# Optimization experiments

Measured on AMD Instinct MI355X. Metric: run time of the kernel, lower is better.

Reference implementation:

```python
import jax, jax.numpy as jnp
import numpy as np

N_NODES = 100000
N_EDGES = 640000
D_IN = 128
D_H = 128


def _lin_params(key, fan_in, fan_out):
    kw, kb = jax.random.split(key)
    s = 1.0 / np.sqrt(fan_in)
    W = jax.random.uniform(kw, (fan_in, fan_out), jnp.float32, -s, s)
    b = jax.random.uniform(kb, (fan_out,), jnp.float32, -s, s)
    return W, b


def setup_inputs() -> dict:
    key = jax.random.key(0)
    ks = jax.random.split(key, 9)
    x = jax.random.normal(ks[0], (N_NODES, D_IN), jnp.float32)
    edge_index = jax.random.randint(ks[1], (2, N_EDGES), 0, N_NODES, dtype=jnp.int64)
    W1, b1 = _lin_params(ks[2], D_IN, D_H)
    W2, b2 = _lin_params(ks[3], D_H, D_H)
    W3, b3 = _lin_params(ks[4], D_H, D_H)
    Wg0, bg0 = _lin_params(ks[5], D_H, D_H)
    Wg1, bg1 = _lin_params(ks[6], D_H, D_H)
    Wo, bo = _lin_params(ks[7], D_H, 1)
    return {"x": x, "edge_index": edge_index,
            "W1": W1, "b1": b1, "W2": W2, "b2": b2, "W3": W3, "b3": b3,
            "Wg0": Wg0, "bg0": bg0, "Wg1": Wg1, "bg1": bg1, "Wo": Wo, "bo": bo}


def gcn_conv(x, src, dst, W, b, n_nodes):
    """PyG GCNConv: D^{-1/2} (A+I) D^{-1/2} X W + b (self-loops added, sym norm)."""
    h = x @ W  # [N, F_out]
    # degree of A+I counted on target side (each self-loop adds 1)
    deg = jnp.zeros((n_nodes,), x.dtype).at[dst].add(1.0) + 1.0
    dis = jax.lax.rsqrt(deg)  # deg^{-1/2}
    coef = dis[src] * dis[dst]  # [E]
    agg = jax.ops.segment_sum(h[src] * coef[:, None], dst, num_segments=n_nodes)
    out = agg + h * (dis * dis)[:, None]  # self-loop term
    return out + b


def reference(x, edge_index, W1, b1, W2, b2, W3, b3, Wg0, bg0, Wg1, bg1, Wo, bo):
    src, dst = edge_index[0], edge_index[1]
    n = x.shape[0]
    lrelu = jax.nn.leaky_relu  # slope 0.01, matches torch default
    # feature extractor MLP
    h = lrelu(x @ W1 + b1)
    h = lrelu(h @ W2 + b2)
    h = lrelu(h @ W3 + b3)
    # input GCN
    h = lrelu(gcn_conv(h, src, dst, Wg0, bg0, n))
    # hidden GCN (dropout is identity in eval mode)
    h = lrelu(gcn_conv(h, src, dst, Wg1, bg1, n))
    # output GCN -> scalar per node
    return gcn_conv(h, src, dst, Wo, bo, n)
```

## Files before the change

kernel.cpp:

```cpp
#include <hip/hip_runtime.h>
#include <hip/hip_bf16.h>

#define D_H 128

typedef __attribute__((ext_vector_type(8))) short bf16x8;
typedef __attribute__((ext_vector_type(4))) float f32x4;

__device__ inline void trunc_split(float x, ushort& hi, ushort& lo) {
    uint u = __builtin_bit_cast(uint, x);
    hi = (ushort)(u >> 16);
    float fh = __builtin_bit_cast(float, u & 0xFFFF0000u);
    float fl = x - fh;
    lo = (ushort)(__builtin_bit_cast(uint, fl) >> 16);
}


__global__ __launch_bounds__(256)
void deg_count_int_kernel(const int* __restrict__ dst, int* __restrict__ cnt, int E) {
    int e = blockIdx.x * 256 + threadIdx.x;
    if (e < E) atomicAdd(&cnt[dst[e]], 1);
}

__global__ __launch_bounds__(256)
void scan_blocks_kernel(const int* __restrict__ cnt, int* __restrict__ rowptr,
                        int* __restrict__ aux, int M) {
    __shared__ int sdata[256];
    const int base = blockIdx.x * 1024 + threadIdx.x * 4;
    int v[4];
#pragma unroll
    for (int i = 0; i < 4; ++i) v[i] = (base + i < M) ? cnt[base + i] : 0;
    int tsum = v[0] + v[1] + v[2] + v[3];
    sdata[threadIdx.x] = tsum;
    __syncthreads();
    int val = tsum;
    for (int off = 1; off < 256; off <<= 1) {
        int n = (threadIdx.x >= off) ? sdata[threadIdx.x - off] : 0;
        __syncthreads();
        val += n;
        sdata[threadIdx.x] = val;
        __syncthreads();
    }
    int run = val - tsum;
#pragma unroll
    for (int i = 0; i < 4; ++i) {
        if (base + i < M) rowptr[base + i] = run;
        run += v[i];
    }
    if (threadIdx.x == 255) aux[blockIdx.x] = val;
}

__global__ __launch_bounds__(128)
void scan_aux_kernel(int* __restrict__ aux, int n) {
    __shared__ int s[128];
    int v = (threadIdx.x < n) ? aux[threadIdx.x] : 0;
    s[threadIdx.x] = v;
    __syncthreads();
    int val = v;
    for (int off = 1; off < 128; off <<= 1) {
        int nn = (threadIdx.x >= off) ? s[threadIdx.x - off] : 0;
        __syncthreads();
        val += nn;
        s[threadIdx.x] = val;
        __syncthreads();
    }
    if (threadIdx.x < n) aux[threadIdx.x] = val - v;
}

__global__ __launch_bounds__(256)
void scan_add_kernel(int* __restrict__ rowptr, int* __restrict__ cursor,
                     const int* __restrict__ aux, const int* __restrict__ cnt,
                     float* __restrict__ dis, int M) {
    int i = blockIdx.x * 256 + threadIdx.x;
    if (i >= M) return;
    int v = rowptr[i] + aux[i >> 10];
    rowptr[i] = v;
    cursor[i] = v;
    dis[i] = rsqrtf((float)cnt[i] + 1.0f);
}

__global__ __launch_bounds__(256)
void scatter_kernel(const int* __restrict__ src, const int* __restrict__ dst,
                    const float* __restrict__ dis, int* __restrict__ cursor,
                    int* __restrict__ es, float* __restrict__ ces, int E) {
    int e = blockIdx.x * 256 + threadIdx.x;
    if (e >= E) return;
    int s = src[e], d = dst[e];
    int pos = atomicAdd(&cursor[d], 1);
    es[pos] = s;
    ces[pos] = dis[s];
}

__global__ __launch_bounds__(256)
void wprep_kernel(const float* __restrict__ W1, const float* __restrict__ W2,
                  const float* __restrict__ W3, const float* __restrict__ W4,
                  const float* __restrict__ W5, ushort* __restrict__ imgs) {
    int w = blockIdx.x >> 6;
    int e = (blockIdx.x & 63) * 256 + threadIdx.x;
    const float* W = w == 0 ? W1 : w == 1 ? W2 : w == 2 ? W3 : w == 3 ? W4 : W5;
    int k = e >> 7, n = e & 127;
    ushort hi, lo;
    trunc_split(W[e], hi, lo);
    ushort* img = imgs + (size_t)w * 34816;
    img[n * 136 + k]         = hi;
    img[17408 + n * 136 + k] = lo;
}

__global__ __launch_bounds__(512, 4)
void fused_mlp4_kernel(const float* __restrict__ X, const ushort* __restrict__ imgs,
                       const float* __restrict__ b1, const float* __restrict__ b2,
                       const float* __restrict__ b3, float* __restrict__ Y, int M) {
    __shared__ ushort sW[34816];
    float* sAct = (float*)sW;

    const int tid  = threadIdx.x;
    const int lane = tid & 63;
    const int wv   = tid >> 6;
    const int bn   = lane & 15;
    const int g    = lane >> 4;
    const int kof  = g * 8;
    const int row0 = blockIdx.x * 128;
    const int lrow = wv * 16 + bn;

    uint4 wreg[9];
    {
        const uint4* g4 = (const uint4*)imgs;
#pragma unroll
        for (int j = 0; j < 9; ++j) {
            int c = j * 512 + tid;
            wreg[j] = (c < 4352) ? g4[c] : make_uint4(0, 0, 0, 0);
        }
    }

    bf16x8 ahi[4], alo[4];
    {
        const int arow = row0 + lrow;
        const bool ok = arow < M;
        const float* ap = X + (size_t)arow * 128 + kof;
#pragma unroll
        for (int kb = 0; kb < 4; ++kb) {
            float f[8];
            if (ok) {
                float4 f0 = *(const float4*)(ap + kb * 32);
                float4 f1 = *(const float4*)(ap + kb * 32 + 4);
                f[0] = f0.x; f[1] = f0.y; f[2] = f0.z; f[3] = f0.w;
                f[4] = f1.x; f[5] = f1.y; f[6] = f1.z; f[7] = f1.w;
            } else {
#pragma unroll
                for (int e = 0; e < 8; ++e) f[e] = 0.f;
            }
            bf16x8 h, l;
#pragma unroll
            for (int e = 0; e < 8; ++e) {
                ushort hb, lb;
                trunc_split(f[e], hb, lb);
                h[e] = (short)hb; l[e] = (short)lb;
            }
            ahi[kb] = h; alo[kb] = l;
        }
    }

    f32x4 acc[8];
    for (int t = 0; t < 4; ++t) {
        {
            uint4* s4 = (uint4*)sW;
#pragma unroll
            for (int j = 0; j < 9; ++j) {
                int c = j * 512 + tid;
                if (c < 4352) s4[c] = wreg[j];
            }
        }
        __syncthreads();

        if (t < 3) {
            const uint4* g4 = (const uint4*)(imgs + (size_t)(t + 1) * 34816);
#pragma unroll
            for (int j = 0; j < 9; ++j) {
                int c = j * 512 + tid;
                wreg[j] = (c < 4352) ? g4[c] : make_uint4(0, 0, 0, 0);
            }
        }

#pragma unroll
        for (int nt = 0; nt < 8; ++nt) acc[nt] = (f32x4){0.f, 0.f, 0.f, 0.f};
#pragma unroll
        for (int kb = 0; kb < 4; ++kb) {
#pragma unroll
            for (int nt = 0; nt < 8; ++nt) {
                const ushort* ph = &sW[(nt * 16 + bn) * 136 + kb * 32 + kof];
                bf16x8 bh = *(const bf16x8*)ph;
                bf16x8 bl = *(const bf16x8*)(ph + 17408);
                acc[nt] = __builtin_amdgcn_mfma_f32_16x16x32_bf16(ahi[kb], bh, acc[nt], 0, 0, 0);
                acc[nt] = __builtin_amdgcn_mfma_f32_16x16x32_bf16(alo[kb], bh, acc[nt], 0, 0, 0);
                acc[nt] = __builtin_amdgcn_mfma_f32_16x16x32_bf16(ahi[kb], bl, acc[nt], 0, 0, 0);
            }
        }

        if (t < 3) {
            __syncthreads();
            const float* bias = t == 0 ? b1 : t == 1 ? b2 : b3;
#pragma unroll
            for (int nt = 0; nt < 8; ++nt) {
                int col = nt * 16 + bn;
                float bc = bias[col];
#pragma unroll
                for (int i = 0; i < 4; ++i) {
                    float v = acc[nt][i] + bc;
                    v = v > 0.f ? v : 0.01f * v;
                    sAct[(wv * 16 + g * 4 + i) * 132 + col] = v;
                }
            }
#pragma unroll
            for (int kb = 0; kb < 4; ++kb) {
                float4 f0 = *(const float4*)&sAct[lrow * 132 + kb * 32 + kof];
                float4 f1 = *(const float4*)&sAct[lrow * 132 + kb * 32 + kof + 4];
                float f[8] = {f0.x, f0.y, f0.z, f0.w, f1.x, f1.y, f1.z, f1.w};
                bf16x8 h, l;
#pragma unroll
                for (int e = 0; e < 8; ++e) {
                    ushort hb, lb;
                    trunc_split(f[e], hb, lb);
                    h[e] = (short)hb; l[e] = (short)lb;
                }
                ahi[kb] = h; alo[kb] = l;
            }
            __syncthreads();
        } else {
#pragma unroll
            for (int nt = 0; nt < 8; ++nt) {
                int col = nt * 16 + bn;
#pragma unroll
                for (int i = 0; i < 4; ++i) {
                    int row = row0 + wv * 16 + g * 4 + i;
                    if (row < M) Y[(size_t)row * 128 + col] = acc[nt][i];
                }
            }
        }
    }
}

__global__ __launch_bounds__(512, 4)
void gemm128_mfma_kernel(const float* __restrict__ X, const ushort* __restrict__ img,
                         float* __restrict__ Y, int M) {
    __shared__ ushort sB[34816];

    const int tid  = threadIdx.x;
    const int lane = tid & 63;
    const int wv   = tid >> 6;
    const int bn   = lane & 15;
    const int g    = lane >> 4;
    const int kof  = g * 8;
    const int row0 = blockIdx.x * 128;
    const int arow = row0 + wv * 16 + bn;

    uint4 wreg[9];
    {
        const uint4* g4 = (const uint4*)img;
#pragma unroll
        for (int j = 0; j < 9; ++j) {
            int c = j * 512 + tid;
            wreg[j] = (c < 4352) ? g4[c] : make_uint4(0, 0, 0, 0);
        }
    }

    bf16x8 ahi[4], alo[4];
    {
        const bool ok = arow < M;
        const float* ap = X + (size_t)arow * 128 + kof;
#pragma unroll
        for (int kb = 0; kb < 4; ++kb) {
            float f[8];
            if (ok) {
                float4 f0 = *(const float4*)(ap + kb * 32);
                float4 f1 = *(const float4*)(ap + kb * 32 + 4);
                f[0] = f0.x; f[1] = f0.y; f[2] = f0.z; f[3] = f0.w;
                f[4] = f1.x; f[5] = f1.y; f[6] = f1.z; f[7] = f1.w;
            } else {
#pragma unroll
                for (int e = 0; e < 8; ++e) f[e] = 0.f;
            }
            bf16x8 h, l;
#pragma unroll
            for (int e = 0; e < 8; ++e) {
                ushort hb, lb;
                trunc_split(f[e], hb, lb);
                h[e] = (short)hb; l[e] = (short)lb;
            }
            ahi[kb] = h; alo[kb] = l;
        }
    }

    {
        uint4* s4 = (uint4*)sB;
#pragma unroll
        for (int j = 0; j < 9; ++j) {
            int c = j * 512 + tid;
            if (c < 4352) s4[c] = wreg[j];
        }
    }
    __syncthreads();

    f32x4 acc[8];
#pragma unroll
    for (int nt = 0; nt < 8; ++nt) acc[nt] = (f32x4){0.f, 0.f, 0.f, 0.f};
#pragma unroll
    for (int kb = 0; kb < 4; ++kb) {
#pragma unroll
        for (int nt = 0; nt < 8; ++nt) {
            const ushort* ph = &sB[(nt * 16 + bn) * 136 + kb * 32 + kof];
            bf16x8 bh = *(const bf16x8*)ph;
            bf16x8 bl = *(const bf16x8*)(ph + 17408);
            acc[nt] = __builtin_amdgcn_mfma_f32_16x16x32_bf16(ahi[kb], bh, acc[nt], 0, 0, 0);
            acc[nt] = __builtin_amdgcn_mfma_f32_16x16x32_bf16(alo[kb], bh, acc[nt], 0, 0, 0);
            acc[nt] = __builtin_amdgcn_mfma_f32_16x16x32_bf16(ahi[kb], bl, acc[nt], 0, 0, 0);
        }
    }

#pragma unroll
    for (int nt = 0; nt < 8; ++nt) {
        int col = nt * 16 + bn;
#pragma unroll
        for (int i = 0; i < 4; ++i) {
            int row = row0 + wv * 16 + g * 4 + i;
            if (row < M) Y[(size_t)row * 128 + col] = acc[nt][i];
        }
    }
}

template<int MODE>
__global__ __launch_bounds__(256)
void gcn_agg_csr_kernel(const float* __restrict__ H, const int* __restrict__ es,
                        const float* __restrict__ ces, const int* __restrict__ rowptr,
                        const int* __restrict__ cnt, const float* __restrict__ dis,
                        const float* __restrict__ bias, const float* __restrict__ Wo,
                        float* __restrict__ Y, float* __restrict__ ho, int M) {
    int w    = (blockIdx.x * 256 + threadIdx.x) >> 6;
    int lane = threadIdx.x & 63;
    if (w >= M) return;

    const float dd  = dis[w];
    const int   beg = rowptr[w];
    const int   n   = cnt[w];

    float2 hv = ((const float2*)H)[(size_t)w * 64 + lane];
    float2 acc;
    acc.x = hv.x * dd * dd;
    acc.y = hv.y * dd * dd;

    int j = 0;
    for (; j + 4 <= n; j += 4) {
        int   s0 = es[beg + j],      s1 = es[beg + j + 1];
        int   s2 = es[beg + j + 2],  s3 = es[beg + j + 3];
        float c0 = ces[beg + j] * dd,     c1 = ces[beg + j + 1] * dd;
        float c2 = ces[beg + j + 2] * dd, c3 = ces[beg + j + 3] * dd;
        float2 v0 = ((const float2*)H)[(size_t)s0 * 64 + lane];
        float2 v1 = ((const float2*)H)[(size_t)s1 * 64 + lane];
        float2 v2 = ((const float2*)H)[(size_t)s2 * 64 + lane];
        float2 v3 = ((const float2*)H)[(size_t)s3 * 64 + lane];
        acc.x += c0 * v0.x + c1 * v1.x + c2 * v2.x + c3 * v3.x;
        acc.y += c0 * v0.y + c1 * v1.y + c2 * v2.y + c3 * v3.y;
    }
    for (; j < n; ++j) {
        int   s = es[beg + j];
        float c = ces[beg + j] * dd;
        float2 v = ((const float2*)H)[(size_t)s * 64 + lane];
        acc.x += c * v.x;
        acc.y += c * v.y;
    }

    float2 bb = ((const float2*)bias)[lane];
    acc.x += bb.x; acc.y += bb.y;
    acc.x = acc.x > 0.f ? acc.x : 0.01f * acc.x;
    acc.y = acc.y > 0.f ? acc.y : 0.01f * acc.y;

    if (MODE == 1) {
        ((float2*)Y)[(size_t)w * 64 + lane] = acc;
    } else {
        float2 wv = ((const float2*)Wo)[lane];
        float p = acc.x * wv.x + acc.y * wv.y;
#pragma unroll
        for (int off = 32; off > 0; off >>= 1) p += __shfl_down(p, off, 64);
        if (lane == 0) ho[w] = p;
    }
}

__global__ __launch_bounds__(256)
void out_csr_kernel(const float* __restrict__ ho, const int* __restrict__ es,
                    const float* __restrict__ ces, const int* __restrict__ rowptr,
                    const int* __restrict__ cnt, const float* __restrict__ dis,
                    const float* __restrict__ bo, float* __restrict__ out, int M) {
    int i = blockIdx.x * 256 + threadIdx.x;
    if (i >= M) return;
    float dd  = dis[i];
    float acc = ho[i] * dd * dd;
    int   beg = rowptr[i], n = cnt[i];
    for (int j = 0; j < n; ++j)
        acc += ces[beg + j] * dd * ho[es[beg + j]];
    out[i] = acc + bo[0];
}


extern "C" void kernel_launch(void* const* d_in, const int* in_sizes, int n_in,
                              void* d_out, int out_size, void* d_ws, size_t ws_size,
                              hipStream_t stream) {
    const float* x   = (const float*)d_in[0];
    const int*   ei  = (const int*)d_in[1];
    const float* W1  = (const float*)d_in[2];
    const float* b1  = (const float*)d_in[3];
    const float* W2  = (const float*)d_in[4];
    const float* b2  = (const float*)d_in[5];
    const float* W3  = (const float*)d_in[6];
    const float* b3  = (const float*)d_in[7];
    const float* Wg0 = (const float*)d_in[8];
    const float* bg0 = (const float*)d_in[9];
    const float* Wg1 = (const float*)d_in[10];
    const float* bg1 = (const float*)d_in[11];
    const float* Wo  = (const float*)d_in[12];
    const float* bo  = (const float*)d_in[13];

    const int M = in_sizes[0] / D_H;
    const int E = in_sizes[1] / 2;
    const int* se = ei;
    const int* de = ei + E;

    float*  A      = (float*)d_ws;
    float*  B      = A + (size_t)M * D_H;
    ushort* Wimg   = (ushort*)(B + (size_t)M * D_H);
    float*  dis    = (float*)(Wimg + 5 * 34816);
    float*  ho     = dis + M;
    float*  ces    = ho + M;
    int*    cnt    = (int*)(ces + E);
    int*    rowptr = cnt + M;
    int*    cursor = rowptr + M;
    int*    es     = cursor + M;
    int*    aux    = es + E;

    float* out = (float*)d_out;

    const int nChunks     = (M + 1023) / 1024;
    const int gemm_blocks = (M + 127) / 128;
    const int node_waves  = (M * 64 + 255) / 256;

    hipMemsetAsync(cnt, 0, M * sizeof(int), stream);
    wprep_kernel<<<320, 256, 0, stream>>>(W1, W2, W3, Wg0, Wg1, Wimg);
    deg_count_int_kernel<<<(E + 255) / 256, 256, 0, stream>>>(de, cnt, E);
    scan_blocks_kernel<<<nChunks, 256, 0, stream>>>(cnt, rowptr, aux, M);
    scan_aux_kernel<<<1, 128, 0, stream>>>(aux, nChunks);
    scan_add_kernel<<<(M + 255) / 256, 256, 0, stream>>>(rowptr, cursor, aux, cnt, dis, M);
    scatter_kernel<<<(E + 255) / 256, 256, 0, stream>>>(se, de, dis, cursor, es, ces, E);

    fused_mlp4_kernel<<<gemm_blocks, 512, 0, stream>>>(x, Wimg, b1, b2, b3, B, M);

    gcn_agg_csr_kernel<1><<<node_waves, 256, 0, stream>>>(B, es, ces, rowptr, cnt, dis, bg0, nullptr, A, nullptr, M);

    gemm128_mfma_kernel<<<gemm_blocks, 512, 0, stream>>>(A, Wimg + 4 * 34816, B, M);

    gcn_agg_csr_kernel<2><<<node_waves, 256, 0, stream>>>(B, es, ces, rowptr, cnt, dis, bg1, Wo, nullptr, ho, M);

    out_csr_kernel<<<(M + 255) / 256, 256, 0, stream>>>(ho, es, ces, rowptr, cnt, dis, bo, out, M);
}
```

Before: 345.0 us.

## Aggregate before second GCN GEMM and fuse bias, activation and output projection

Uses linearity of the GCN to reorder the second GCN layer: aggregation runs on the input features first, then the GEMM runs with bias, leaky ReLU and the dot with Wo fused into its epilogue. This writes only a per-node scalar instead of a full 128-wide matrix and drops the separate reduction in the aggregation kernel. Weight staging in both GEMM kernels is also simplified to load directly into shared memory, with no register prefetch. That gives up the overlap of weight loads with compute in the fused MLP. Shuffle-based row reductions replace the full output store.

```diff
diff --git a/kernel.cpp b/kernel.cpp
--- a/kernel.cpp
+++ b/kernel.cpp
@@ -121,16 +121,6 @@
     const int row0 = blockIdx.x * 128;
     const int lrow = wv * 16 + bn;
 
-    uint4 wreg[9];
-    {
-        const uint4* g4 = (const uint4*)imgs;
-#pragma unroll
-        for (int j = 0; j < 9; ++j) {
-            int c = j * 512 + tid;
-            wreg[j] = (c < 4352) ? g4[c] : make_uint4(0, 0, 0, 0);
-        }
-    }
-
     bf16x8 ahi[4], alo[4];
     {
         const int arow = row0 + lrow;
@@ -162,23 +152,15 @@
     f32x4 acc[8];
     for (int t = 0; t < 4; ++t) {
         {
-            uint4* s4 = (uint4*)sW;
+            const uint4* g4 = (const uint4*)(imgs + (size_t)t * 34816);
+            uint4*       s4 = (uint4*)sW;
 #pragma unroll
             for (int j = 0; j < 9; ++j) {
                 int c = j * 512 + tid;
-                if (c < 4352) s4[c] = wreg[j];
+                if (c < 4352) s4[c] = g4[c];
             }
         }
         __syncthreads();
-
-        if (t < 3) {
-            const uint4* g4 = (const uint4*)(imgs + (size_t)(t + 1) * 34816);
-#pragma unroll
-            for (int j = 0; j < 9; ++j) {
-                int c = j * 512 + tid;
-                wreg[j] = (c < 4352) ? g4[c] : make_uint4(0, 0, 0, 0);
-            }
-        }
 
 #pragma unroll
         for (int nt = 0; nt < 8; ++nt) acc[nt] = (f32x4){0.f, 0.f, 0.f, 0.f};
@@ -239,8 +221,9 @@
 }
 
 __global__ __launch_bounds__(512, 4)
-void gemm128_mfma_kernel(const float* __restrict__ X, const ushort* __restrict__ img,
-                         float* __restrict__ Y, int M) {
+void gemm_ho_kernel(const float* __restrict__ X, const ushort* __restrict__ img,
+                    const float* __restrict__ bias, const float* __restrict__ Wo,
+                    float* __restrict__ ho, int M) {
     __shared__ ushort sB[34816];
 
     const int tid  = threadIdx.x;
@@ -252,13 +235,13 @@
     const int row0 = blockIdx.x * 128;
     const int arow = row0 + wv * 16 + bn;
 
-    uint4 wreg[9];
     {
         const uint4* g4 = (const uint4*)img;
+        uint4*       s4 = (uint4*)sB;
 #pragma unroll
         for (int j = 0; j < 9; ++j) {
             int c = j * 512 + tid;
-            wreg[j] = (c < 4352) ? g4[c] : make_uint4(0, 0, 0, 0);
+            if (c < 4352) s4[c] = g4[c];
         }
     }
 
@@ -288,15 +271,6 @@
             ahi[kb] = h; alo[kb] = l;
         }
     }
-
-    {
-        uint4* s4 = (uint4*)sB;
-#pragma unroll
-        for (int j = 0; j < 9; ++j) {
-            int c = j * 512 + tid;
-            if (c < 4352) s4[c] = wreg[j];
-        }
-    }
     __syncthreads();
 
     f32x4 acc[8];
@@ -315,13 +289,29 @@
         }
     }
 
+    float part[4] = {0.f, 0.f, 0.f, 0.f};
 #pragma unroll
     for (int nt = 0; nt < 8; ++nt) {
         int col = nt * 16 + bn;
+        float bc = bias[col];
+        float wo = Wo[col];
+#pragma unroll
+        for (int i = 0; i < 4; ++i) {
+            float v = acc[nt][i] + bc;
+            v = v > 0.f ? v : 0.01f * v;
+            part[i] += v * wo;
+        }
+    }
+#pragma unroll
+    for (int m = 1; m < 16; m <<= 1) {
+#pragma unroll
+        for (int i = 0; i < 4; ++i) part[i] += __shfl_xor(part[i], m, 64);
+    }
+    if (bn == 0) {
 #pragma unroll
         for (int i = 0; i < 4; ++i) {
             int row = row0 + wv * 16 + g * 4 + i;
-            if (row < M) Y[(size_t)row * 128 + col] = acc[nt][i];
+            if (row < M) ho[row] = part[i];
         }
     }
 }
@@ -331,8 +321,7 @@
 void gcn_agg_csr_kernel(const float* __restrict__ H, const int* __restrict__ es,
                         const float* __restrict__ ces, const int* __restrict__ rowptr,
                         const int* __restrict__ cnt, const float* __restrict__ dis,
-                        const float* __restrict__ bias, const float* __restrict__ Wo,
-                        float* __restrict__ Y, float* __restrict__ ho, int M) {
+                        const float* __restrict__ bias, float* __restrict__ Y, int M) {
     int w    = (blockIdx.x * 256 + threadIdx.x) >> 6;
     int lane = threadIdx.x & 63;
     if (w >= M) return;
@@ -367,20 +356,13 @@
         acc.y += c * v.y;
     }
 
-    float2 bb = ((const float2*)bias)[lane];
-    acc.x += bb.x; acc.y += bb.y;
-    acc.x = acc.x > 0.f ? acc.x : 0.01f * acc.x;
-    acc.y = acc.y > 0.f ? acc.y : 0.01f * acc.y;
-
     if (MODE == 1) {
-        ((float2*)Y)[(size_t)w * 64 + lane] = acc;
-    } else {
-        float2 wv = ((const float2*)Wo)[lane];
-        float p = acc.x * wv.x + acc.y * wv.y;
-#pragma unroll
-        for (int off = 32; off > 0; off >>= 1) p += __shfl_down(p, off, 64);
-        if (lane == 0) ho[w] = p;
-    }
+        float2 bb = ((const float2*)bias)[lane];
+        acc.x += bb.x; acc.y += bb.y;
+        acc.x = acc.x > 0.f ? acc.x : 0.01f * acc.x;
+        acc.y = acc.y > 0.f ? acc.y : 0.01f * acc.y;
+    }
+    ((float2*)Y)[(size_t)w * 64 + lane] = acc;
 }
 
 __global__ __launch_bounds__(256)
@@ -450,11 +432,10 @@
 
     fused_mlp4_kernel<<<gemm_blocks, 512, 0, stream>>>(x, Wimg, b1, b2, b3, B, M);
 
-    gcn_agg_csr_kernel<1><<<node_waves, 256, 0, stream>>>(B, es, ces, rowptr, cnt, dis, bg0, nullptr, A, nullptr, M);
-
-    gemm128_mfma_kernel<<<gemm_blocks, 512, 0, stream>>>(A, Wimg + 4 * 34816, B, M);
-
-    gcn_agg_csr_kernel<2><<<node_waves, 256, 0, stream>>>(B, es, ces, rowptr, cnt, dis, bg1, Wo, nullptr, ho, M);
+    gcn_agg_csr_kernel<1><<<node_waves, 256, 0, stream>>>(B, es, ces, rowptr, cnt, dis, bg0, A, M);
+
+    gcn_agg_csr_kernel<0><<<node_waves, 256, 0, stream>>>(A, es, ces, rowptr, cnt, dis, nullptr, B, M);
+    gemm_ho_kernel<<<gemm_blocks, 512, 0, stream>>>(B, Wimg + 4 * 34816, bg1, Wo, ho, M);
 
     out_csr_kernel<<<(M + 255) / 256, 256, 0, stream>>>(ho, es, ces, rowptr, cnt, dis, bo, out, M);
 }
```

Result: faster. 291.8 us (-15.4%).
